# Kernel optimization log

Hardware: AMD Instinct MI355X
Metric: run time of the kernel (lower is better)

The kernel has to match this reference:

```python
import jax, jax.numpy as jnp
import numpy as np

N = 6144
IN_DIM = 512
CHANNELS = 4
C_DIM = 64
ITERATIONS = 3
BETA = 1.0
EDGE_P = 0.005  # ~30 avg degree


def _l2norm(x):
    # F.normalize(dim=-1): x / max(||x||_2, eps)
    return x / jnp.maximum(jnp.linalg.norm(x, axis=-1, keepdims=True), 1e-12)


def setup_inputs() -> dict:
    key = jax.random.key(0)
    kf, ka, kw, kb = jax.random.split(key, 4)
    features = jax.random.normal(kf, (N, IN_DIM), dtype=jnp.float32)
    # sparse 0/1 adjacency, densified (module calls adj.to_dense())
    adj = (jax.random.uniform(ka, (N, N)) < EDGE_P).astype(jnp.int32)
    # per-channel weights/biases, init ~ N(0, 1) as in init_parameters
    W = jax.random.normal(kw, (CHANNELS, IN_DIM, C_DIM), dtype=jnp.float32)
    b = jax.random.normal(kb, (CHANNELS, 1, C_DIM), dtype=jnp.float32)
    return {"features": features, "adj": adj, "W": W, "b": b}


def reference(features, adj, W, b):
    mask = adj > 0  # [N, N]
    # per-channel projection + row L2-normalize -> [C, N, K]
    feats = _l2norm(jnp.einsum('nd,cdk->cnk', features, W) + b)
    for _ in range(ITERATIONS):
        # per-channel dense self-attention scores, masked by adjacency
        att = jnp.einsum('cnk,cmk->cnm', feats, feats) / BETA  # [C, N, N]
        att = jnp.where(mask[None, :, :], att, 0.0)
        # softmax across channels (torch dim=2 after cat == channel axis)
        att = jax.nn.softmax(att, axis=0)
        att = jnp.where(mask[None, :, :], att, 0.0)
        # aggregate and renormalize
        feats = _l2norm(feats + jnp.einsum('cnm,cmk->cnk', att, feats))
    # concat channels along feature dim -> [N, C*K]
    return jnp.transpose(feats, (1, 0, 2)).reshape(N, CHANNELS * C_DIM)
```

## Files before the change

### kernel.cpp

```cpp
#include <hip/hip_runtime.h>
#include <hip/hip_bf16.h>
#include <math.h>

#define NN      6144
#define IN_DIM  512
#define CH      4
#define CDIM    64
#define NODE    (CH * CDIM)
#define PR      16
#define MAXD    96

typedef int  v4i __attribute__((ext_vector_type(4)));

__global__ __launch_bounds__(256) void proj_kernel(
    const float* __restrict__ feat,
    const float* __restrict__ W,
    const float* __restrict__ bias,
    float* __restrict__ out)
{
    __shared__ float lds[PR * IN_DIM];
    const int t    = threadIdx.x;
    const int row0 = blockIdx.x * PR;

    {
        const float4* src = (const float4*)(feat + (size_t)row0 * IN_DIM);
        float4* dst = (float4*)lds;
#pragma unroll
        for (int i = 0; i < (PR * IN_DIM / 4) / 256; ++i)
            dst[t + i * 256] = src[t + i * 256];
    }
    __syncthreads();

    const int g  = t >> 6;
    const int q  = t & 63;
    const int c  = q >> 4;
    const int k0 = (q & 15) * 4;

    float acc[4][4];
#pragma unroll
    for (int r = 0; r < 4; ++r)
#pragma unroll
        for (int j = 0; j < 4; ++j) acc[r][j] = 0.0f;

    const float* Wc   = W + (size_t)c * IN_DIM * CDIM + k0;
    const float* arow = lds + g * 4 * IN_DIM;

    for (int d = 0; d < IN_DIM; d += 4) {
        const float4 w0 = *(const float4*)(Wc + (size_t)(d + 0) * CDIM);
        const float4 w1 = *(const float4*)(Wc + (size_t)(d + 1) * CDIM);
        const float4 w2 = *(const float4*)(Wc + (size_t)(d + 2) * CDIM);
        const float4 w3 = *(const float4*)(Wc + (size_t)(d + 3) * CDIM);
#pragma unroll
        for (int r = 0; r < 4; ++r) {
            const float4 a = *(const float4*)(arow + r * IN_DIM + d);
            acc[r][0] = fmaf(a.x, w0.x, fmaf(a.y, w1.x, fmaf(a.z, w2.x, fmaf(a.w, w3.x, acc[r][0]))));
            acc[r][1] = fmaf(a.x, w0.y, fmaf(a.y, w1.y, fmaf(a.z, w2.y, fmaf(a.w, w3.y, acc[r][1]))));
            acc[r][2] = fmaf(a.x, w0.z, fmaf(a.y, w1.z, fmaf(a.z, w2.z, fmaf(a.w, w3.z, acc[r][2]))));
            acc[r][3] = fmaf(a.x, w0.w, fmaf(a.y, w1.w, fmaf(a.z, w2.w, fmaf(a.w, w3.w, acc[r][3]))));
        }
    }

    const float4 bv = *(const float4*)(bias + c * CDIM + k0);
#pragma unroll
    for (int r = 0; r < 4; ++r) {
        acc[r][0] += bv.x; acc[r][1] += bv.y; acc[r][2] += bv.z; acc[r][3] += bv.w;
    }

#pragma unroll
    for (int r = 0; r < 4; ++r) {
        float ss = acc[r][0] * acc[r][0] + acc[r][1] * acc[r][1]
                 + acc[r][2] * acc[r][2] + acc[r][3] * acc[r][3];
        ss += __shfl_xor(ss, 1, 64);
        ss += __shfl_xor(ss, 2, 64);
        ss += __shfl_xor(ss, 4, 64);
        ss += __shfl_xor(ss, 8, 64);
        const float rn = __builtin_amdgcn_rsqf(fmaxf(ss, 1e-24f));
        float4 res = make_float4(acc[r][0] * rn, acc[r][1] * rn, acc[r][2] * rn, acc[r][3] * rn);
        *(float4*)(out + (size_t)(row0 + g * 4 + r) * NODE + c * CDIM + k0) = res;
    }
}

__global__ __launch_bounds__(256) void ell_kernel(
    const int* __restrict__ adj,
    int* __restrict__ deg,
    int* __restrict__ cols)
{
    __shared__ int cnt;
    const int n = blockIdx.x;
    if (threadIdx.x == 0) cnt = 0;
    __syncthreads();

    const v4i* row = (const v4i*)(adj + (size_t)n * NN);
    int* rowcols = cols + (size_t)n * MAXD;
    for (int i = threadIdx.x; i < NN / 4; i += 256) {
        const v4i v = __builtin_nontemporal_load(&row[i]);
        if (v.x | v.y | v.z | v.w) {
            const int base = i * 4;
            if (v.x) { int p = atomicAdd(&cnt, 1); if (p < MAXD) rowcols[p] = base + 0; }
            if (v.y) { int p = atomicAdd(&cnt, 1); if (p < MAXD) rowcols[p] = base + 1; }
            if (v.z) { int p = atomicAdd(&cnt, 1); if (p < MAXD) rowcols[p] = base + 2; }
            if (v.w) { int p = atomicAdd(&cnt, 1); if (p < MAXD) rowcols[p] = base + 3; }
        }
    }
    __syncthreads();
    if (threadIdx.x == 0) deg[n] = min(cnt, MAXD);
}

__global__ __launch_bounds__(256) void iter_kernel(
    const float* __restrict__ fin,
    float* __restrict__ fout,
    const int* __restrict__ deg,
    const int* __restrict__ cols)
{
    const int wv   = threadIdx.x >> 6;
    const int lane = threadIdx.x & 63;
    const int n    = blockIdx.x * 4 + wv;

    const float4* fin4 = (const float4*)fin;
    const float4 q = fin4[(size_t)n * 64 + lane];
    float4 acc = q;

    const int d = deg[n];
    const int* cl = cols + (size_t)n * MAXD;
    const int nch = d >> 2;

    int4   mm;
    float4 f0, f1, f2, f3;
    if (nch > 0) {
        mm = *(const int4*)cl;
        f0 = fin4[(size_t)mm.x * 64 + lane];
        f1 = fin4[(size_t)mm.y * 64 + lane];
        f2 = fin4[(size_t)mm.z * 64 + lane];
        f3 = fin4[(size_t)mm.w * 64 + lane];
    }

    for (int ch = 0; ch < nch; ++ch) {
        int4   mn;
        float4 g0, g1, g2, g3;
        const bool more = (ch + 1 < nch);
        if (more) {
            mn = *(const int4*)(cl + (ch + 1) * 4);
            g0 = fin4[(size_t)mn.x * 64 + lane];
            g1 = fin4[(size_t)mn.y * 64 + lane];
            g2 = fin4[(size_t)mn.z * 64 + lane];
            g3 = fin4[(size_t)mn.w * 64 + lane];
        }

        float p0 = fmaf(q.x, f0.x, fmaf(q.y, f0.y, fmaf(q.z, f0.z, q.w * f0.w)));
        float p1 = fmaf(q.x, f1.x, fmaf(q.y, f1.y, fmaf(q.z, f1.z, q.w * f1.w)));
        float p2 = fmaf(q.x, f2.x, fmaf(q.y, f2.y, fmaf(q.z, f2.z, q.w * f2.w)));
        float p3 = fmaf(q.x, f3.x, fmaf(q.y, f3.y, fmaf(q.z, f3.z, q.w * f3.w)));
#pragma unroll
        for (int off = 1; off <= 8; off <<= 1) {
            p0 += __shfl_xor(p0, off, 64);
            p1 += __shfl_xor(p1, off, 64);
            p2 += __shfl_xor(p2, off, 64);
            p3 += __shfl_xor(p3, off, 64);
        }
        const float e0 = __expf(p0);
        const float e1 = __expf(p1);
        const float e2 = __expf(p2);
        const float e3 = __expf(p3);
        float s0 = e0 + __shfl_xor(e0, 16, 64);
        float s1 = e1 + __shfl_xor(e1, 16, 64);
        float s2 = e2 + __shfl_xor(e2, 16, 64);
        float s3 = e3 + __shfl_xor(e3, 16, 64);
        s0 += __shfl_xor(s0, 32, 64);
        s1 += __shfl_xor(s1, 32, 64);
        s2 += __shfl_xor(s2, 32, 64);
        s3 += __shfl_xor(s3, 32, 64);
        const float w0 = e0 * __builtin_amdgcn_rcpf(s0);
        const float w1 = e1 * __builtin_amdgcn_rcpf(s1);
        const float w2 = e2 * __builtin_amdgcn_rcpf(s2);
        const float w3 = e3 * __builtin_amdgcn_rcpf(s3);

        acc.x = fmaf(w0, f0.x, fmaf(w1, f1.x, fmaf(w2, f2.x, fmaf(w3, f3.x, acc.x))));
        acc.y = fmaf(w0, f0.y, fmaf(w1, f1.y, fmaf(w2, f2.y, fmaf(w3, f3.y, acc.y))));
        acc.z = fmaf(w0, f0.z, fmaf(w1, f1.z, fmaf(w2, f2.z, fmaf(w3, f3.z, acc.z))));
        acc.w = fmaf(w0, f0.w, fmaf(w1, f1.w, fmaf(w2, f2.w, fmaf(w3, f3.w, acc.w))));

        if (more) { f0 = g0; f1 = g1; f2 = g2; f3 = g3; }
    }

    for (int i = nch * 4; i < d; ++i) {
        const int m = cl[i];
        const float4 f = fin4[(size_t)m * 64 + lane];
        float p = fmaf(q.x, f.x, fmaf(q.y, f.y, fmaf(q.z, f.z, q.w * f.w)));
        p += __shfl_xor(p, 1, 64);
        p += __shfl_xor(p, 2, 64);
        p += __shfl_xor(p, 4, 64);
        p += __shfl_xor(p, 8, 64);
        const float e = __expf(p);
        float s = e + __shfl_xor(e, 16, 64);
        s += __shfl_xor(s, 32, 64);
        const float w = e * __builtin_amdgcn_rcpf(s);
        acc.x = fmaf(w, f.x, acc.x);
        acc.y = fmaf(w, f.y, acc.y);
        acc.z = fmaf(w, f.z, acc.z);
        acc.w = fmaf(w, f.w, acc.w);
    }

    float ss = fmaf(acc.x, acc.x, fmaf(acc.y, acc.y, fmaf(acc.z, acc.z, acc.w * acc.w)));
    ss += __shfl_xor(ss, 1, 64);
    ss += __shfl_xor(ss, 2, 64);
    ss += __shfl_xor(ss, 4, 64);
    ss += __shfl_xor(ss, 8, 64);
    const float rn = __builtin_amdgcn_rsqf(fmaxf(ss, 1e-24f));
    acc.x *= rn; acc.y *= rn; acc.z *= rn; acc.w *= rn;

    ((float4*)fout)[(size_t)n * 64 + lane] = acc;
}

extern "C" void kernel_launch(void* const* d_in, const int* in_sizes, int n_in,
                              void* d_out, int out_size, void* d_ws, size_t ws_size,
                              hipStream_t stream) {
    const float* features = (const float*)d_in[0];
    const int*   adj      = (const int*)d_in[1];
    const float* W        = (const float*)d_in[2];
    const float* b        = (const float*)d_in[3];
    float* out = (float*)d_out;

    float* featsA = (float*)d_ws;
    float* featsB = featsA + (size_t)NN * NODE;
    int*   deg    = (int*)(featsB + (size_t)NN * NODE);
    int*   cols   = deg + NN;

    proj_kernel<<<NN / PR, 256, 0, stream>>>(features, W, b, featsA);
    ell_kernel<<<NN, 256, 0, stream>>>(adj, deg, cols);
    iter_kernel<<<NN / 4, 256, 0, stream>>>(featsA, featsB, deg, cols);
    iter_kernel<<<NN / 4, 256, 0, stream>>>(featsB, featsA, deg, cols);
    iter_kernel<<<NN / 4, 256, 0, stream>>>(featsA, out, deg, cols);
}
```

Baseline: 319.8 us.

## Merge projection and ELL build into one launch; remap iter lanes per neighbor

Projection and adjacency-to-ELL conversion now run in a single launch, with block index choosing the role, so the two independent stages overlap and one launch disappears. The projection tile shrinks to 8 rows per block to make more blocks. The iteration kernel now processes four neighbors at once: each 16-lane group handles one neighbor and each lane holds 16 consecutive floats (one channel quarter). This shortens the shuffle reductions and removes the scalar remainder loop, at the cost of a final cross-group reduction of 16 accumulators and predicated padding for partial chunks.

```diff
diff --git a/kernel.cpp b/kernel.cpp
--- a/kernel.cpp
+++ b/kernel.cpp
@@ -7,103 +7,99 @@
 #define CH      4
 #define CDIM    64
 #define NODE    (CH * CDIM)
-#define PR      16
+#define PR      8
+#define PBLK    (NN / PR)
 #define MAXD    96
 
-typedef int  v4i __attribute__((ext_vector_type(4)));
-
-__global__ __launch_bounds__(256) void proj_kernel(
+typedef int v4i __attribute__((ext_vector_type(4)));
+
+__global__ __launch_bounds__(256) void proj_ell_kernel(
     const float* __restrict__ feat,
     const float* __restrict__ W,
     const float* __restrict__ bias,
-    float* __restrict__ out)
+    const int*   __restrict__ adj,
+    float* __restrict__ out,
+    int*   __restrict__ deg,
+    int*   __restrict__ cols)
 {
     __shared__ float lds[PR * IN_DIM];
-    const int t    = threadIdx.x;
-    const int row0 = blockIdx.x * PR;
-
-    {
-        const float4* src = (const float4*)(feat + (size_t)row0 * IN_DIM);
-        float4* dst = (float4*)lds;
-#pragma unroll
-        for (int i = 0; i < (PR * IN_DIM / 4) / 256; ++i)
-            dst[t + i * 256] = src[t + i * 256];
+    const int t = threadIdx.x;
+
+    if (blockIdx.x < PBLK) {
+        const int row0 = blockIdx.x * PR;
+        {
+            const float4* src = (const float4*)(feat + (size_t)row0 * IN_DIM);
+            float4* dst = (float4*)lds;
+#pragma unroll
+            for (int i = 0; i < (PR * IN_DIM / 4) / 256; ++i)
+                dst[t + i * 256] = src[t + i * 256];
+        }
+        __syncthreads();
+
+        const int g  = t >> 6;
+        const int q  = t & 63;
+        const int c  = q >> 4;
+        const int k0 = (q & 15) * 4;
+
+        float acc[2][4];
+#pragma unroll
+        for (int r = 0; r < 2; ++r)
+#pragma unroll
+            for (int j = 0; j < 4; ++j) acc[r][j] = 0.0f;
+
+        const float* Wc   = W + (size_t)c * IN_DIM * CDIM + k0;
+        const float* arow = lds + g * 2 * IN_DIM;
+
+        for (int d = 0; d < IN_DIM; d += 4) {
+            const float4 w0 = *(const float4*)(Wc + (size_t)(d + 0) * CDIM);
+            const float4 w1 = *(const float4*)(Wc + (size_t)(d + 1) * CDIM);
+            const float4 w2 = *(const float4*)(Wc + (size_t)(d + 2) * CDIM);
+            const float4 w3 = *(const float4*)(Wc + (size_t)(d + 3) * CDIM);
+#pragma unroll
+            for (int r = 0; r < 2; ++r) {
+                const float4 a = *(const float4*)(arow + r * IN_DIM + d);
+                acc[r][0] = fmaf(a.x, w0.x, fmaf(a.y, w1.x, fmaf(a.z, w2.x, fmaf(a.w, w3.x, acc[r][0]))));
+                acc[r][1] = fmaf(a.x, w0.y, fmaf(a.y, w1.y, fmaf(a.z, w2.y, fmaf(a.w, w3.y, acc[r][1]))));
+                acc[r][2] = fmaf(a.x, w0.z, fmaf(a.y, w1.z, fmaf(a.z, w2.z, fmaf(a.w, w3.z, acc[r][2]))));
+                acc[r][3] = fmaf(a.x, w0.w, fmaf(a.y, w1.w, fmaf(a.z, w2.w, fmaf(a.w, w3.w, acc[r][3]))));
+            }
+        }
+
+        const float4 bv = *(const float4*)(bias + c * CDIM + k0);
+#pragma unroll
+        for (int r = 0; r < 2; ++r) {
+            acc[r][0] += bv.x; acc[r][1] += bv.y; acc[r][2] += bv.z; acc[r][3] += bv.w;
+            float ss = acc[r][0] * acc[r][0] + acc[r][1] * acc[r][1]
+                     + acc[r][2] * acc[r][2] + acc[r][3] * acc[r][3];
+            ss += __shfl_xor(ss, 1, 64);
+            ss += __shfl_xor(ss, 2, 64);
+            ss += __shfl_xor(ss, 4, 64);
+            ss += __shfl_xor(ss, 8, 64);
+            const float rn = __builtin_amdgcn_rsqf(fmaxf(ss, 1e-24f));
+            float4 res = make_float4(acc[r][0] * rn, acc[r][1] * rn, acc[r][2] * rn, acc[r][3] * rn);
+            *(float4*)(out + (size_t)(row0 + g * 2 + r) * NODE + c * CDIM + k0) = res;
+        }
+    } else {
+        int* cnt = (int*)lds;
+        const int n = blockIdx.x - PBLK;
+        if (t == 0) *cnt = 0;
+        __syncthreads();
+
+        const v4i* row = (const v4i*)(adj + (size_t)n * NN);
+        int* rowcols = cols + (size_t)n * MAXD;
+        for (int i = t; i < NN / 4; i += 256) {
+            const v4i v = __builtin_nontemporal_load(&row[i]);
+            if (v.x | v.y | v.z | v.w) {
+                const int base = i * 4;
+                if (v.x) { int p = atomicAdd(cnt, 1); if (p < MAXD) rowcols[p] = base + 0; }
+                if (v.y) { int p = atomicAdd(cnt, 1); if (p < MAXD) rowcols[p] = base + 1; }
+                if (v.z) { int p = atomicAdd(cnt, 1); if (p < MAXD) rowcols[p] = base + 2; }
+                if (v.w) { int p = atomicAdd(cnt, 1); if (p < MAXD) rowcols[p] = base + 3; }
+            }
+        }
+        __syncthreads();
+        if (t == 0) deg[n] = min(*cnt, MAXD);
     }
-    __syncthreads();
-
-    const int g  = t >> 6;
-    const int q  = t & 63;
-    const int c  = q >> 4;
-    const int k0 = (q & 15) * 4;
-
-    float acc[4][4];
-#pragma unroll
-    for (int r = 0; r < 4; ++r)
-#pragma unroll
-        for (int j = 0; j < 4; ++j) acc[r][j] = 0.0f;
-
-    const float* Wc   = W + (size_t)c * IN_DIM * CDIM + k0;
-    const float* arow = lds + g * 4 * IN_DIM;
-
-    for (int d = 0; d < IN_DIM; d += 4) {
-        const float4 w0 = *(const float4*)(Wc + (size_t)(d + 0) * CDIM);
-        const float4 w1 = *(const float4*)(Wc + (size_t)(d + 1) * CDIM);
-        const float4 w2 = *(const float4*)(Wc + (size_t)(d + 2) * CDIM);
-        const float4 w3 = *(const float4*)(Wc + (size_t)(d + 3) * CDIM);
-#pragma unroll
-        for (int r = 0; r < 4; ++r) {
-            const float4 a = *(const float4*)(arow + r * IN_DIM + d);
-            acc[r][0] = fmaf(a.x, w0.x, fmaf(a.y, w1.x, fmaf(a.z, w2.x, fmaf(a.w, w3.x, acc[r][0]))));
-            acc[r][1] = fmaf(a.x, w0.y, fmaf(a.y, w1.y, fmaf(a.z, w2.y, fmaf(a.w, w3.y, acc[r][1]))));
-            acc[r][2] = fmaf(a.x, w0.z, fmaf(a.y, w1.z, fmaf(a.z, w2.z, fmaf(a.w, w3.z, acc[r][2]))));
-            acc[r][3] = fmaf(a.x, w0.w, fmaf(a.y, w1.w, fmaf(a.z, w2.w, fmaf(a.w, w3.w, acc[r][3]))));
-        }
-    }
-
-    const float4 bv = *(const float4*)(bias + c * CDIM + k0);
-#pragma unroll
-    for (int r = 0; r < 4; ++r) {
-        acc[r][0] += bv.x; acc[r][1] += bv.y; acc[r][2] += bv.z; acc[r][3] += bv.w;
-    }
-
-#pragma unroll
-    for (int r = 0; r < 4; ++r) {
-        float ss = acc[r][0] * acc[r][0] + acc[r][1] * acc[r][1]
-                 + acc[r][2] * acc[r][2] + acc[r][3] * acc[r][3];
-        ss += __shfl_xor(ss, 1, 64);
-        ss += __shfl_xor(ss, 2, 64);
-        ss += __shfl_xor(ss, 4, 64);
-        ss += __shfl_xor(ss, 8, 64);
-        const float rn = __builtin_amdgcn_rsqf(fmaxf(ss, 1e-24f));
-        float4 res = make_float4(acc[r][0] * rn, acc[r][1] * rn, acc[r][2] * rn, acc[r][3] * rn);
-        *(float4*)(out + (size_t)(row0 + g * 4 + r) * NODE + c * CDIM + k0) = res;
-    }
-}
-
-__global__ __launch_bounds__(256) void ell_kernel(
-    const int* __restrict__ adj,
-    int* __restrict__ deg,
-    int* __restrict__ cols)
-{
-    __shared__ int cnt;
-    const int n = blockIdx.x;
-    if (threadIdx.x == 0) cnt = 0;
-    __syncthreads();
-
-    const v4i* row = (const v4i*)(adj + (size_t)n * NN);
-    int* rowcols = cols + (size_t)n * MAXD;
-    for (int i = threadIdx.x; i < NN / 4; i += 256) {
-        const v4i v = __builtin_nontemporal_load(&row[i]);
-        if (v.x | v.y | v.z | v.w) {
-            const int base = i * 4;
-            if (v.x) { int p = atomicAdd(&cnt, 1); if (p < MAXD) rowcols[p] = base + 0; }
-            if (v.y) { int p = atomicAdd(&cnt, 1); if (p < MAXD) rowcols[p] = base + 1; }
-            if (v.z) { int p = atomicAdd(&cnt, 1); if (p < MAXD) rowcols[p] = base + 2; }
-            if (v.w) { int p = atomicAdd(&cnt, 1); if (p < MAXD) rowcols[p] = base + 3; }
-        }
-    }
-    __syncthreads();
-    if (threadIdx.x == 0) deg[n] = min(cnt, MAXD);
 }
 
 __global__ __launch_bounds__(256) void iter_kernel(
@@ -115,100 +111,85 @@
     const int wv   = threadIdx.x >> 6;
     const int lane = threadIdx.x & 63;
     const int n    = blockIdx.x * 4 + wv;
-
-    const float4* fin4 = (const float4*)fin;
-    const float4 q = fin4[(size_t)n * 64 + lane];
-    float4 acc = q;
+    const int nb   = lane >> 4;
+    const int cj   = lane & 15;
+
+    const float4* qp = (const float4*)(fin + (size_t)n * NODE + cj * 16);
+    const float4 q0 = qp[0], q1 = qp[1], q2 = qp[2], q3 = qp[3];
+    float4 a0 = make_float4(0.f, 0.f, 0.f, 0.f), a1 = a0, a2 = a0, a3 = a0;
 
     const int d = deg[n];
     const int* cl = cols + (size_t)n * MAXD;
-    const int nch = d >> 2;
-
-    int4   mm;
+    const int nch = (d + 3) >> 2;
+
+    bool val = nb < d;
     float4 f0, f1, f2, f3;
-    if (nch > 0) {
-        mm = *(const int4*)cl;
-        f0 = fin4[(size_t)mm.x * 64 + lane];
-        f1 = fin4[(size_t)mm.y * 64 + lane];
-        f2 = fin4[(size_t)mm.z * 64 + lane];
-        f3 = fin4[(size_t)mm.w * 64 + lane];
+    {
+        const int m = val ? cl[nb] : 0;
+        const float4* fp = (const float4*)(fin + (size_t)m * NODE + cj * 16);
+        f0 = fp[0]; f1 = fp[1]; f2 = fp[2]; f3 = fp[3];
     }
 
     for (int ch = 0; ch < nch; ++ch) {
-        int4   mn;
+        const bool more = (ch + 1 < nch);
+        bool val2 = false;
         float4 g0, g1, g2, g3;
-        const bool more = (ch + 1 < nch);
         if (more) {
-            mn = *(const int4*)(cl + (ch + 1) * 4);
-            g0 = fin4[(size_t)mn.x * 64 + lane];
-            g1 = fin4[(size_t)mn.y * 64 + lane];
-            g2 = fin4[(size_t)mn.z * 64 + lane];
-            g3 = fin4[(size_t)mn.w * 64 + lane];
-        }
-
-        float p0 = fmaf(q.x, f0.x, fmaf(q.y, f0.y, fmaf(q.z, f0.z, q.w * f0.w)));
-        float p1 = fmaf(q.x, f1.x, fmaf(q.y, f1.y, fmaf(q.z, f1.z, q.w * f1.w)));
-        float p2 = fmaf(q.x, f2.x, fmaf(q.y, f2.y, fmaf(q.z, f2.z, q.w * f2.w)));
-        float p3 = fmaf(q.x, f3.x, fmaf(q.y, f3.y, fmaf(q.z, f3.z, q.w * f3.w)));
-#pragma unroll
-        for (int off = 1; off <= 8; off <<= 1) {
-            p0 += __shfl_xor(p0, off, 64);
-            p1 += __shfl_xor(p1, off, 64);
-            p2 += __shfl_xor(p2, off, 64);
-            p3 += __shfl_xor(p3, off, 64);
-        }
-        const float e0 = __expf(p0);
-        const float e1 = __expf(p1);
-        const float e2 = __expf(p2);
-        const float e3 = __expf(p3);
-        float s0 = e0 + __shfl_xor(e0, 16, 64);
-        float s1 = e1 + __shfl_xor(e1, 16, 64);
-        float s2 = e2 + __shfl_xor(e2, 16, 64);
-        float s3 = e3 + __shfl_xor(e3, 16, 64);
-        s0 += __shfl_xor(s0, 32, 64);
-        s1 += __shfl_xor(s1, 32, 64);
-        s2 += __shfl_xor(s2, 32, 64);
-        s3 += __shfl_xor(s3, 32, 64);
-        const float w0 = e0 * __builtin_amdgcn_rcpf(s0);
-        const float w1 = e1 * __builtin_amdgcn_rcpf(s1);
-        const float w2 = e2 * __builtin_amdgcn_rcpf(s2);
-        const float w3 = e3 * __builtin_amdgcn_rcpf(s3);
-
-        acc.x = fmaf(w0, f0.x, fmaf(w1, f1.x, fmaf(w2, f2.x, fmaf(w3, f3.x, acc.x))));
-        acc.y = fmaf(w0, f0.y, fmaf(w1, f1.y, fmaf(w2, f2.y, fmaf(w3, f3.y, acc.y))));
-        acc.z = fmaf(w0, f0.z, fmaf(w1, f1.z, fmaf(w2, f2.z, fmaf(w3, f3.z, acc.z))));
-        acc.w = fmaf(w0, f0.w, fmaf(w1, f1.w, fmaf(w2, f2.w, fmaf(w3, f3.w, acc.w))));
-
-        if (more) { f0 = g0; f1 = g1; f2 = g2; f3 = g3; }
-    }
-
-    for (int i = nch * 4; i < d; ++i) {
-        const int m = cl[i];
-        const float4 f = fin4[(size_t)m * 64 + lane];
-        float p = fmaf(q.x, f.x, fmaf(q.y, f.y, fmaf(q.z, f.z, q.w * f.w)));
+            const int mg2 = (ch + 1) * 4 + nb;
+            val2 = mg2 < d;
+            const int m2 = val2 ? cl[mg2] : 0;
+            const float4* gp = (const float4*)(fin + (size_t)m2 * NODE + cj * 16);
+            g0 = gp[0]; g1 = gp[1]; g2 = gp[2]; g3 = gp[3];
+        }
+
+        float p = fmaf(q0.x, f0.x, fmaf(q0.y, f0.y, fmaf(q0.z, f0.z, q0.w * f0.w)));
+        p = fmaf(q1.x, f1.x, fmaf(q1.y, f1.y, fmaf(q1.z, f1.z, fmaf(q1.w, f1.w, p))));
+        p = fmaf(q2.x, f2.x, fmaf(q2.y, f2.y, fmaf(q2.z, f2.z, fmaf(q2.w, f2.w, p))));
+        p = fmaf(q3.x, f3.x, fmaf(q3.y, f3.y, fmaf(q3.z, f3.z, fmaf(q3.w, f3.w, p))));
         p += __shfl_xor(p, 1, 64);
         p += __shfl_xor(p, 2, 64);
-        p += __shfl_xor(p, 4, 64);
-        p += __shfl_xor(p, 8, 64);
         const float e = __expf(p);
-        float s = e + __shfl_xor(e, 16, 64);
-        s += __shfl_xor(s, 32, 64);
-        const float w = e * __builtin_amdgcn_rcpf(s);
-        acc.x = fmaf(w, f.x, acc.x);
-        acc.y = fmaf(w, f.y, acc.y);
-        acc.z = fmaf(w, f.z, acc.z);
-        acc.w = fmaf(w, f.w, acc.w);
+        float s = e + __shfl_xor(e, 4, 64);
+        s += __shfl_xor(s, 8, 64);
+        const float w = val ? e * __builtin_amdgcn_rcpf(s) : 0.0f;
+
+        a0.x = fmaf(w, f0.x, a0.x); a0.y = fmaf(w, f0.y, a0.y);
+        a0.z = fmaf(w, f0.z, a0.z); a0.w = fmaf(w, f0.w, a0.w);
+        a1.x = fmaf(w, f1.x, a1.x); a1.y = fmaf(w, f1.y, a1.y);
+        a1.z = fmaf(w, f1.z, a1.z); a1.w = fmaf(w, f1.w, a1.w);
+        a2.x = fmaf(w, f2.x, a2.x); a2.y = fmaf(w, f2.y, a2.y);
+        a2.z = fmaf(w, f2.z, a2.z); a2.w = fmaf(w, f2.w, a2.w);
+        a3.x = fmaf(w, f3.x, a3.x); a3.y = fmaf(w, f3.y, a3.y);
+        a3.z = fmaf(w, f3.z, a3.z); a3.w = fmaf(w, f3.w, a3.w);
+
+        if (more) { f0 = g0; f1 = g1; f2 = g2; f3 = g3; val = val2; }
     }
 
-    float ss = fmaf(acc.x, acc.x, fmaf(acc.y, acc.y, fmaf(acc.z, acc.z, acc.w * acc.w)));
+#define RED_NB(X) X += __shfl_xor(X, 16, 64); X += __shfl_xor(X, 32, 64)
+    RED_NB(a0.x); RED_NB(a0.y); RED_NB(a0.z); RED_NB(a0.w);
+    RED_NB(a1.x); RED_NB(a1.y); RED_NB(a1.z); RED_NB(a1.w);
+    RED_NB(a2.x); RED_NB(a2.y); RED_NB(a2.z); RED_NB(a2.w);
+    RED_NB(a3.x); RED_NB(a3.y); RED_NB(a3.z); RED_NB(a3.w);
+#undef RED_NB
+    a0.x += q0.x; a0.y += q0.y; a0.z += q0.z; a0.w += q0.w;
+    a1.x += q1.x; a1.y += q1.y; a1.z += q1.z; a1.w += q1.w;
+    a2.x += q2.x; a2.y += q2.y; a2.z += q2.z; a2.w += q2.w;
+    a3.x += q3.x; a3.y += q3.y; a3.z += q3.z; a3.w += q3.w;
+
+    float ss = a0.x * a0.x + a0.y * a0.y + a0.z * a0.z + a0.w * a0.w
+             + a1.x * a1.x + a1.y * a1.y + a1.z * a1.z + a1.w * a1.w
+             + a2.x * a2.x + a2.y * a2.y + a2.z * a2.z + a2.w * a2.w
+             + a3.x * a3.x + a3.y * a3.y + a3.z * a3.z + a3.w * a3.w;
     ss += __shfl_xor(ss, 1, 64);
     ss += __shfl_xor(ss, 2, 64);
-    ss += __shfl_xor(ss, 4, 64);
-    ss += __shfl_xor(ss, 8, 64);
     const float rn = __builtin_amdgcn_rsqf(fmaxf(ss, 1e-24f));
-    acc.x *= rn; acc.y *= rn; acc.z *= rn; acc.w *= rn;
-
-    ((float4*)fout)[(size_t)n * 64 + lane] = acc;
+    a0.x *= rn; a0.y *= rn; a0.z *= rn; a0.w *= rn;
+    a1.x *= rn; a1.y *= rn; a1.z *= rn; a1.w *= rn;
+    a2.x *= rn; a2.y *= rn; a2.z *= rn; a2.w *= rn;
+    a3.x *= rn; a3.y *= rn; a3.z *= rn; a3.w *= rn;
+
+    const float4 v = (nb == 0) ? a0 : (nb == 1) ? a1 : (nb == 2) ? a2 : a3;
+    *(float4*)(fout + (size_t)n * NODE + cj * 16 + nb * 4) = v;
 }
 
 extern "C" void kernel_launch(void* const* d_in, const int* in_sizes, int n_in,
@@ -225,8 +206,8 @@
     int*   deg    = (int*)(featsB + (size_t)NN * NODE);
     int*   cols   = deg + NN;
 
-    proj_kernel<<<NN / PR, 256, 0, stream>>>(features, W, b, featsA);
-    ell_kernel<<<NN, 256, 0, stream>>>(adj, deg, cols);
+    proj_ell_kernel<<<PBLK + NN, 256, 0, stream>>>(features, W, b, adj,
+                                                   featsA, deg, cols);
     iter_kernel<<<NN / 4, 256, 0, stream>>>(featsA, featsB, deg, cols);
     iter_kernel<<<NN / 4, 256, 0, stream>>>(featsB, featsA, deg, cols);
     iter_kernel<<<NN / 4, 256, 0, stream>>>(featsA, out, deg, cols);
```

Measured after the change: 331.6 us. +3.7%, slower.
